# Kernel tuning notes

Hardware: AMD Instinct MI355X
Metric: run time of the kernel (lower is better)

Reference implementation:

```python
import jax, jax.numpy as jnp
import numpy as np


def _gcn(G, A, x, W, b):
    # G: (K,N,N) chebyshev supports, A: (B,N,N) attention, x: (B,N,p)
    s = jnp.einsum('kij,bjp->bkip', G, x)          # graph conv per cheb order
    s = jnp.einsum('bij,bkjp->bikp', A, s)         # attention bmm, -> (B,N,K,p)
    B, N, K, p = s.shape
    s = s.reshape(B, N, K * p)                     # concat over k (k-major blocks)
    return s @ W + b


def setup_inputs() -> dict:
    key = jax.random.key(0)
    ks = jax.random.split(key, 8)
    B, T, N, C = 16, 12, 1024, 1
    K, H = 3, 64
    din = C + H  # 65
    x = jax.random.normal(ks[0], (B, T, N, C), dtype=jnp.float32)
    G = jax.random.normal(ks[1], (K, N, N), dtype=jnp.float32) / np.sqrt(N)
    A = jax.random.uniform(ks[2], (B, N, N), dtype=jnp.float32) / N
    W_gate = jax.random.normal(ks[3], (K * din, 2 * H), dtype=jnp.float32) * 0.02
    b_gate = jnp.zeros((2 * H,), dtype=jnp.float32)
    W_update = jax.random.normal(ks[4], (K * din, H), dtype=jnp.float32) * 0.02
    b_update = jnp.zeros((H,), dtype=jnp.float32)
    W_dec = jax.random.normal(ks[5], (H, 12 * 1), dtype=jnp.float32) * 0.02
    b_dec = jnp.zeros((12,), dtype=jnp.float32)
    return {"x": x, "G": G, "A": A, "W_gate": W_gate, "b_gate": b_gate,
            "W_update": W_update, "b_update": b_update, "W_dec": W_dec, "b_dec": b_dec}


def reference(x, G, A, W_gate, b_gate, W_update, b_update, W_dec, b_dec):
    B, T, N, _ = x.shape
    H = W_update.shape[1]
    out_steps, output_dim = 12, 1

    def step(h, xt):
        combined = jnp.concatenate([xt, h], axis=-1)              # (B,N,din)
        zr = jax.nn.sigmoid(_gcn(G, A, combined, W_gate, b_gate))  # (B,N,2H)
        z, r = zr[..., :H], zr[..., H:]
        cand = jnp.concatenate([xt, r * h], axis=-1)
        hc = jnp.tanh(_gcn(G, A, cand, W_update, b_update))
        h_new = z * hc + (1.0 - z) * h
        return h_new, None

    h0 = jnp.zeros((B, N, H), dtype=x.dtype)
    h_last, _ = jax.lax.scan(step, h0, jnp.swapaxes(x, 0, 1))      # scan over T
    out = h_last @ W_dec + b_dec                                   # (B,N,out_steps*output_dim)
    out = out.reshape(B, N, out_steps, output_dim)
    return jnp.transpose(out, (0, 2, 1, 3))                        # (B,out_steps,N,output_dim)
```

## Files before the change

kernel.cpp:

```cpp
#include <hip/hip_runtime.h>

#define B_  16
#define T_  12
#define N_  1024
#define K_  3
#define H_  64
#define DIN 65
#define KH  192
#define OG  128

typedef _Float16 f16x4 __attribute__((ext_vector_type(4)));
typedef _Float16 f16x8 __attribute__((ext_vector_type(8)));
typedef float    f32x4 __attribute__((ext_vector_type(4)));

static const size_t OFF_H   = 0;
static const size_t OFF_ZB  = 1048576;
static const size_t OFF_S2  = 2097152;
static const size_t OFF_HTA = 2686976;
static const size_t OFF_HTB = 3211264;
static const size_t OFF_S1  = 3735552;
static const size_t OFF_WGT = 4030464;
static const size_t OFF_WUT = 4042752;
static const size_t OFF_WX  = 4048896;
static const size_t OFF_GT  = 4049472;
static const size_t OFF_AG  = 5622336;
static const size_t OFF_AF  = 30788160;

__global__ __launch_bounds__(256) void k_repack(const float* __restrict__ Wg,
                                                const float* __restrict__ Wu,
                                                _Float16* __restrict__ wghT,
                                                _Float16* __restrict__ wuhT,
                                                float* __restrict__ wx) {
    const float inv = 1.0f / 1024.0f;
    int idx = blockIdx.x * 256 + threadIdx.x;
    if (idx < 128 * 192) {
        int o = idx / 192, d = idx % 192;
        int k = d / 64, c = d % 64;
        wghT[idx] = (_Float16)(Wg[(size_t)(k * DIN + 1 + c) * OG + o] * inv);
    } else if (idx < 128 * 192 + 64 * 192) {
        int j = idx - 128 * 192;
        int o = j / 192, d = j % 192;
        int k = d / 64, c = d % 64;
        wuhT[j] = (_Float16)(Wu[(size_t)(k * DIN + 1 + c) * H_ + o] * inv);
    } else if (idx < 128 * 192 + 64 * 192 + 576) {
        int j = idx - 128 * 192 - 64 * 192;
        if (j < 384) { int k = j >> 7, o = j & 127; wx[j] = Wg[(size_t)(k * DIN) * OG + o] * inv; }
        else { int j2 = j - 384; int k = j2 >> 6, o = j2 & 63; wx[j] = Wu[(size_t)(k * DIN) * H_ + o] * inv; }
    }
}

__global__ __launch_bounds__(256) void k_acvt(const float* __restrict__ A,
                                              _Float16* __restrict__ Af) {
    size_t idx = ((size_t)blockIdx.x * 256 + threadIdx.x) * 8;
    float4 a = *(const float4*)&A[idx];
    float4 c = *(const float4*)&A[idx + 4];
    f16x8 v = {(_Float16)(a.x*1024.f), (_Float16)(a.y*1024.f), (_Float16)(a.z*1024.f), (_Float16)(a.w*1024.f),
               (_Float16)(c.x*1024.f), (_Float16)(c.y*1024.f), (_Float16)(c.z*1024.f), (_Float16)(c.w*1024.f)};
    *(f16x8*)&Af[idx] = v;
}

__global__ __launch_bounds__(256) void k_gtr(const float* __restrict__ G,
                                             _Float16* __restrict__ GfT) {
    int bx = blockIdx.x;
    int kk = bx >> 8, rem = bx & 255, ti = rem >> 4, tj = rem & 15;
    int i0 = ti * 64, j0 = tj * 64;
    __shared__ _Float16 s[64][72];
    int tid = threadIdx.x;
    int r = tid >> 2, cb = (tid & 3) * 16;
    const float* Gp = G + ((size_t)kk << 20) + ((size_t)(i0 + r) << 10) + j0 + cb;
    #pragma unroll
    for (int q = 0; q < 4; ++q) {
        float4 v = *(const float4*)&Gp[q * 4];
        f16x4 hv = {(_Float16)v.x, (_Float16)v.y, (_Float16)v.z, (_Float16)v.w};
        *(f16x4*)&s[r][cb + q * 4] = hv;
    }
    __syncthreads();
    alignas(16) _Float16 tmp[16];
    #pragma unroll
    for (int q = 0; q < 16; ++q) tmp[q] = s[cb + q][r];
    _Float16* outp = GfT + ((size_t)kk << 20) + ((size_t)(j0 + r) << 10) + i0 + cb;
    *(f16x8*)&outp[0] = *(f16x8*)&tmp[0];
    *(f16x8*)&outp[8] = *(f16x8*)&tmp[8];
}

__global__ __launch_bounds__(256) void k_ag(const _Float16* __restrict__ Af,
                                            const _Float16* __restrict__ GfT,
                                            _Float16* __restrict__ AG) {
    int bxr = blockIdx.x;
    int bx = (bxr & 7) * 384 + (bxr >> 3);
    int inst = bx >> 6, tile = bx & 63;
    int b = inst / 3, kk = inst % 3;
    int i0 = (tile >> 3) * 128, j0 = (tile & 7) * 128;
    __shared__ _Float16 sA[2][128][72], sB[2][128][72];
    int tid = threadIdx.x;
    int w = tid >> 6, lane = tid & 63, ln = lane & 15, kg = lane >> 4;
    int mq = (w & 1) * 64, nq = (w >> 1) * 64;
    int srow = tid >> 1, cb = (tid & 1) * 32;
    const _Float16* qa = Af  + ((size_t)b << 20)  + ((size_t)(i0 + srow) << 10) + cb;
    const _Float16* qb = GfT + ((size_t)kk << 20) + ((size_t)(j0 + srow) << 10) + cb;

    f32x4 acc[4][4];
    #pragma unroll
    for (int mt = 0; mt < 4; ++mt)
        #pragma unroll
        for (int nt = 0; nt < 4; ++nt) acc[mt][nt] = (f32x4){0.f, 0.f, 0.f, 0.f};

    f16x8 ra[4], rb[4];
    #pragma unroll
    for (int q = 0; q < 4; ++q) { ra[q] = *(const f16x8*)&qa[q * 8]; rb[q] = *(const f16x8*)&qb[q * 8]; }
    #pragma unroll
    for (int q = 0; q < 4; ++q) {
        *(f16x8*)&sA[0][srow][cb + q * 8] = ra[q];
        *(f16x8*)&sB[0][srow][cb + q * 8] = rb[q];
    }
    __syncthreads();

    for (int tt = 0; tt < 16; ++tt) {
        int cur = tt & 1;
        if (tt < 15) {
            int kn = (tt + 1) * 64;
            #pragma unroll
            for (int q = 0; q < 4; ++q) { ra[q] = *(const f16x8*)&qa[kn + q * 8]; rb[q] = *(const f16x8*)&qb[kn + q * 8]; }
        }
        #pragma unroll
        for (int ks = 0; ks < 2; ++ks) {
            int ko = ks * 32 + kg * 8;
            f16x8 a[4], bfr[4];
            #pragma unroll
            for (int mt = 0; mt < 4; ++mt) a[mt] = *(const f16x8*)&sA[cur][mq + mt * 16 + ln][ko];
            #pragma unroll
            for (int nt = 0; nt < 4; ++nt) bfr[nt] = *(const f16x8*)&sB[cur][nq + nt * 16 + ln][ko];
            #pragma unroll
            for (int mt = 0; mt < 4; ++mt)
                #pragma unroll
                for (int nt = 0; nt < 4; ++nt)
                    acc[mt][nt] = __builtin_amdgcn_mfma_f32_16x16x32_f16(a[mt], bfr[nt], acc[mt][nt], 0, 0, 0);
        }
        if (tt < 15) {
            int nb = cur ^ 1;
            #pragma unroll
            for (int q = 0; q < 4; ++q) {
                *(f16x8*)&sA[nb][srow][cb + q * 8] = ra[q];
                *(f16x8*)&sB[nb][srow][cb + q * 8] = rb[q];
            }
            __syncthreads();
        }
    }

    _Float16* outp = AG + ((size_t)(b * 3 + kk) << 20);
    #pragma unroll
    for (int mt = 0; mt < 4; ++mt)
        #pragma unroll
        for (int r = 0; r < 4; ++r) {
            int i = i0 + mq + mt * 16 + kg * 4 + r;
            #pragma unroll
            for (int nt = 0; nt < 4; ++nt) {
                int j = j0 + nq + nt * 16 + ln;
                outp[((size_t)i << 10) + j] = (_Float16)acc[mt][nt][r];
            }
        }
}

__global__ __launch_bounds__(256) void k_s1b(const float* __restrict__ G,
                                             const float* __restrict__ x,
                                             _Float16* __restrict__ S1) {
    int bx = blockIdx.x;
    int nh = bx & 1, it = (bx >> 1) & 15, kk = bx >> 5;
    int i0 = it * 64, m0 = nh * 96;
    __shared__ _Float16 sA[64][72], sB[96][72];
    int tid = threadIdx.x, wid = tid >> 6, ln = tid & 15, kl = (tid & 63) >> 4;
    const float* Gk = G + (size_t)kk * N_ * N_;
    f32x4 acc[6];
    #pragma unroll
    for (int n = 0; n < 6; ++n) acc[n] = (f32x4){0.f, 0.f, 0.f, 0.f};
    for (int kc = 0; kc < N_; kc += 64) {
        #pragma unroll
        for (int it2 = 0; it2 < 4; ++it2) {
            int idx = it2 * 256 + tid; int row = idx >> 4, c4 = (idx & 15) * 4;
            float4 g = *(const float4*)&Gk[(size_t)(i0 + row) * N_ + kc + c4];
            f16x4 hv = {(_Float16)g.x, (_Float16)g.y, (_Float16)g.z, (_Float16)g.w};
            *(f16x4*)&sA[row][c4] = hv;
        }
        #pragma unroll
        for (int it2 = 0; it2 < 6; ++it2) {
            int idx = it2 * 256 + tid; int row = idx >> 4, c4 = (idx & 15) * 4;
            float4 g = *(const float4*)&x[(size_t)(m0 + row) * N_ + kc + c4];
            f16x4 hv = {(_Float16)g.x, (_Float16)g.y, (_Float16)g.z, (_Float16)g.w};
            *(f16x4*)&sB[row][c4] = hv;
        }
        __syncthreads();
        #pragma unroll
        for (int ks = 0; ks < 4; ++ks) {
            int ko = ks * 16 + kl * 4;
            f16x4 a = *(const f16x4*)&sA[wid * 16 + ln][ko];
            #pragma unroll
            for (int n = 0; n < 6; ++n) {
                f16x4 b = *(const f16x4*)&sB[n * 16 + ln][ko];
                acc[n] = __builtin_amdgcn_mfma_f32_16x16x16f16(a, b, acc[n], 0, 0, 0);
            }
        }
        __syncthreads();
    }
    #pragma unroll
    for (int n = 0; n < 6; ++n) {
        int m = m0 + n * 16 + ln;
        #pragma unroll
        for (int r = 0; r < 4; ++r) {
            int i = i0 + wid * 16 + kl * 4 + r;
            S1[(((size_t)kk * 192 + m) << 10) + i] = (_Float16)acc[n][r];
        }
    }
}

__global__ __launch_bounds__(256) void k_s2b(const _Float16* __restrict__ Af,
                                             const _Float16* __restrict__ S1,
                                             float* __restrict__ S2) {
    int bx = blockIdx.x; int it = bx & 15, b = bx >> 4; int i0 = it * 64;
    __shared__ _Float16 sA[64][72], sB[48][72];
    int tid = threadIdx.x, wid = tid >> 6, ln = tid & 15, kl = (tid & 63) >> 4;
    f32x4 acc[3];
    #pragma unroll
    for (int n = 0; n < 3; ++n) acc[n] = (f32x4){0.f, 0.f, 0.f, 0.f};
    for (int kc = 0; kc < N_; kc += 64) {
        #pragma unroll
        for (int it2 = 0; it2 < 2; ++it2) {
            int idx = it2 * 256 + tid; int row = idx >> 3, c8 = (idx & 7) * 8;
            *(uint4*)&sA[row][c8] = *(const uint4*)&Af[((size_t)b << 20) + ((size_t)(i0 + row) << 10) + kc + c8];
        }
        for (int idx = tid; idx < 288; idx += 256) {
            int row = idx >> 3, c8 = (idx & 7) * 8;
            int kq = row / 12, tq = row - kq * 12;
            *(uint4*)&sB[row][c8] = *(const uint4*)&S1[(((size_t)kq * 192 + b * T_ + tq) << 10) + kc + c8];
        }
        __syncthreads();
        #pragma unroll
        for (int ks = 0; ks < 4; ++ks) {
            int ko = ks * 16 + kl * 4;
            f16x4 a = *(const f16x4*)&sA[wid * 16 + ln][ko];
            #pragma unroll
            for (int n = 0; n < 3; ++n) {
                f16x4 b = *(const f16x4*)&sB[n * 16 + ln][ko];
                acc[n] = __builtin_amdgcn_mfma_f32_16x16x16f16(a, b, acc[n], 0, 0, 0);
            }
        }
        __syncthreads();
    }
    #pragma unroll
    for (int n = 0; n < 3; ++n) {
        int col = n * 16 + ln;
        if (col < 36) {
            int kq = col / 12, tq = col - kq * 12;
            #pragma unroll
            for (int r = 0; r < 4; ++r) {
                int i = i0 + wid * 16 + kl * 4 + r;
                S2[(((size_t)(b * 3 + kq) * T_ + tq) << 10) + i] = acc[n][r];
            }
        }
    }
}

__global__ __launch_bounds__(256) void k_fzr(const _Float16* __restrict__ AG,
                                             const _Float16* __restrict__ HtIn,
                                             const _Float16* __restrict__ wghT,
                                             const float* __restrict__ wx,
                                             const float* __restrict__ bg,
                                             const float* __restrict__ S2,
                                             const float* __restrict__ h,
                                             float* __restrict__ zb,
                                             _Float16* __restrict__ HtOut, int t) {
    int bx = blockIdx.x; int it = bx & 63, b = bx >> 6; int i0 = it * 16;
    __shared__ __align__(16) char smem[32256];
    _Float16 (*sA)[48][72] = reinterpret_cast<_Float16(*)[48][72]>(smem);
    _Float16 (*sB)[64][72] = reinterpret_cast<_Float16(*)[64][72]>(smem + 13824);
    _Float16 (*sZ)[200]    = reinterpret_cast<_Float16(*)[200]>(smem);
    _Float16 (*sW)[72]     = reinterpret_cast<_Float16(*)[72]>(smem + 6400);
    __shared__ float sS2[3][16];
    __shared__ float sWX[384];
    __shared__ float sBias[128];
    int tid = threadIdx.x;
    int w = tid >> 6, lane = tid & 63, ln = lane & 15, kg = lane >> 4;
    if (tid < 48) { int k = tid >> 4, il = tid & 15; sS2[k][il] = S2[(((size_t)(b * 3 + k) * T_ + t) << 10) + i0 + il]; }
    for (int q = tid; q < 384; q += 256) sWX[q] = wx[q];
    if (tid < 128) sBias[tid] = bg[tid];

    const _Float16* pA[3]; int c4A[3], rowA[3];
    #pragma unroll
    for (int q = 0; q < 3; ++q) {
        int idx = q * 256 + tid; rowA[q] = idx >> 4; c4A[q] = (idx & 15) * 4;
        int kb = rowA[q] >> 4, rloc = rowA[q] & 15;
        pA[q] = AG + ((size_t)(b * 3 + kb) << 20) + ((size_t)(i0 + rloc) << 10) + c4A[q];
    }
    const _Float16* pB[2]; int c8B[2], rowB[2];
    #pragma unroll
    for (int q = 0; q < 2; ++q) {
        int idx = q * 256 + tid; rowB[q] = idx >> 3; c8B[q] = (idx & 7) * 8;
        pB[q] = HtIn + ((size_t)b << 16) + ((size_t)rowB[q] << 10) + c8B[q];
    }

    f32x4 acc[3];
    #pragma unroll
    for (int n = 0; n < 3; ++n) acc[n] = (f32x4){0.f, 0.f, 0.f, 0.f};

    f16x4 ra[3]; f16x8 rb[2];
    #pragma unroll
    for (int q = 0; q < 3; ++q) ra[q] = *(const f16x4*)pA[q];
    #pragma unroll
    for (int q = 0; q < 2; ++q) rb[q] = *(const f16x8*)pB[q];
    #pragma unroll
    for (int q = 0; q < 3; ++q) *(f16x4*)&sA[0][rowA[q]][c4A[q]] = ra[q];
    #pragma unroll
    for (int q = 0; q < 2; ++q) *(f16x8*)&sB[0][rowB[q]][c8B[q]] = rb[q];
    __syncthreads();

    int kbF = (w * 3) >> 2, kbL = (w * 3 + 2) >> 2;
    for (int tt = 0; tt < 16; ++tt) {
        int cur = tt & 1;
        if (tt < 15) {
            int kn = (tt + 1) * 64;
            #pragma unroll
            for (int q = 0; q < 3; ++q) ra[q] = *(const f16x4*)&pA[q][kn];
            #pragma unroll
            for (int q = 0; q < 2; ++q) rb[q] = *(const f16x8*)&pB[q][kn];
        }
        #pragma unroll
        for (int ks = 0; ks < 2; ++ks) {
            int ko = ks * 32 + kg * 8;
            f16x8 aF = *(const f16x8*)&sA[cur][kbF * 16 + ln][ko];
            f16x8 aL = *(const f16x8*)&sA[cur][kbL * 16 + ln][ko];
            #pragma unroll
            for (int ni = 0; ni < 3; ++ni) {
                int ct = w * 3 + ni;
                f16x8 bb = *(const f16x8*)&sB[cur][(ct & 3) * 16 + ln][ko];
                f16x8 a = ((ct >> 2) != kbF) ? aL : aF;
                acc[ni] = __builtin_amdgcn_mfma_f32_16x16x32_f16(a, bb, acc[ni], 0, 0, 0);
            }
        }
        if (tt < 15) {
            int nb = cur ^ 1;
            #pragma unroll
            for (int q = 0; q < 3; ++q) *(f16x4*)&sA[nb][rowA[q]][c4A[q]] = ra[q];
            #pragma unroll
            for (int q = 0; q < 2; ++q) *(f16x8*)&sB[nb][rowB[q]][c8B[q]] = rb[q];
            __syncthreads();
        }
    }
    __syncthreads();

    #pragma unroll
    for (int ni = 0; ni < 3; ++ni)
        #pragma unroll
        for (int r = 0; r < 4; ++r)
            sZ[kg * 4 + r][(w * 3 + ni) * 16 + ln] = (_Float16)acc[ni][r];

    f32x4 e[2];
    e[0] = (f32x4){0.f, 0.f, 0.f, 0.f};
    e[1] = (f32x4){0.f, 0.f, 0.f, 0.f};
    for (int kc = 0; kc < 192; kc += 64) {
        #pragma unroll
        for (int it2 = 0; it2 < 4; ++it2) {
            int idx = it2 * 256 + tid; int row = idx >> 3, c8 = (idx & 7) * 8;
            *(f16x8*)&sW[row][c8] = *(const f16x8*)&wghT[(size_t)row * 192 + kc + c8];
        }
        __syncthreads();
        #pragma unroll
        for (int ks = 0; ks < 4; ++ks) {
            int ko = ks * 16 + kg * 4;
            f16x4 az  = *(const f16x4*)&sZ[ln][kc + ko];
            f16x4 bw0 = *(const f16x4*)&sW[w * 32 + ln][ko];
            f16x4 bw1 = *(const f16x4*)&sW[w * 32 + 16 + ln][ko];
            e[0] = __builtin_amdgcn_mfma_f32_16x16x16f16(az, bw0, e[0], 0, 0, 0);
            e[1] = __builtin_amdgcn_mfma_f32_16x16x16f16(az, bw1, e[1], 0, 0, 0);
        }
        __syncthreads();
    }

    #pragma unroll
    for (int n = 0; n < 2; ++n) {
        int o = w * 32 + n * 16 + ln;
        float w0 = sWX[o], w1 = sWX[128 + o], w2 = sWX[256 + o], bi = sBias[o];
        if (o < H_) {
            #pragma unroll
            for (int r = 0; r < 4; ++r) {
                int il = kg * 4 + r;
                float pre = e[n][r] + w0 * sS2[0][il] + w1 * sS2[1][il] + w2 * sS2[2][il] + bi;
                float v = 1.0f / (1.0f + expf(-pre));
                zb[((size_t)((b << 10) + i0 + il)) * H_ + o] = v;
            }
        } else {
            int c = o - H_;
            alignas(8) _Float16 hb[4];
            #pragma unroll
            for (int r = 0; r < 4; ++r) {
                int il = kg * 4 + r;
                float pre = e[n][r] + w0 * sS2[0][il] + w1 * sS2[1][il] + w2 * sS2[2][il] + bi;
                float v = 1.0f / (1.0f + expf(-pre));
                hb[r] = (_Float16)(v * h[((size_t)((b << 10) + i0 + il)) * H_ + c]);
            }
            *(f16x4*)&HtOut[((size_t)(b * 64 + c) << 10) + i0 + kg * 4] = *(f16x4*)&hb[0];
        }
    }
}

__global__ __launch_bounds__(256) void k_fup(const _Float16* __restrict__ AG,
                                             const _Float16* __restrict__ HtIn,
                                             const _Float16* __restrict__ wuhT,
                                             const float* __restrict__ wx,
                                             const float* __restrict__ bu,
                                             const float* __restrict__ S2,
                                             const float* __restrict__ zb,
                                             float* __restrict__ h,
                                             _Float16* __restrict__ HtOut, int t) {
    int bx = blockIdx.x; int it = bx & 63, b = bx >> 6; int i0 = it * 16;
    __shared__ __align__(16) char smem[32256];
    _Float16 (*sA)[48][72] = reinterpret_cast<_Float16(*)[48][72]>(smem);
    _Float16 (*sB)[64][72] = reinterpret_cast<_Float16(*)[64][72]>(smem + 13824);
    _Float16 (*sZ)[200]    = reinterpret_cast<_Float16(*)[200]>(smem);
    _Float16 (*sW)[72]     = reinterpret_cast<_Float16(*)[72]>(smem + 6400);
    __shared__ float sS2[3][16];
    __shared__ float sWX[192];
    __shared__ float sBias[64];
    int tid = threadIdx.x;
    int w = tid >> 6, lane = tid & 63, ln = lane & 15, kg = lane >> 4;
    if (tid < 48) { int k = tid >> 4, il = tid & 15; sS2[k][il] = S2[(((size_t)(b * 3 + k) * T_ + t) << 10) + i0 + il]; }
    if (tid < 192) sWX[tid] = wx[384 + tid];
    if (tid < 64) sBias[tid] = bu[tid];

    const _Float16* pA[3]; int c4A[3], rowA[3];
    #pragma unroll
    for (int q = 0; q < 3; ++q) {
        int idx = q * 256 + tid; rowA[q] = idx >> 4; c4A[q] = (idx & 15) * 4;
        int kb = rowA[q] >> 4, rloc = rowA[q] & 15;
        pA[q] = AG + ((size_t)(b * 3 + kb) << 20) + ((size_t)(i0 + rloc) << 10) + c4A[q];
    }
    const _Float16* pB[2]; int c8B[2], rowB[2];
    #pragma unroll
    for (int q = 0; q < 2; ++q) {
        int idx = q * 256 + tid; rowB[q] = idx >> 3; c8B[q] = (idx & 7) * 8;
        pB[q] = HtIn + ((size_t)b << 16) + ((size_t)rowB[q] << 10) + c8B[q];
    }

    f32x4 acc[3];
    #pragma unroll
    for (int n = 0; n < 3; ++n) acc[n] = (f32x4){0.f, 0.f, 0.f, 0.f};

    f16x4 ra[3]; f16x8 rb[2];
    #pragma unroll
    for (int q = 0; q < 3; ++q) ra[q] = *(const f16x4*)pA[q];
    #pragma unroll
    for (int q = 0; q < 2; ++q) rb[q] = *(const f16x8*)pB[q];
    #pragma unroll
    for (int q = 0; q < 3; ++q) *(f16x4*)&sA[0][rowA[q]][c4A[q]] = ra[q];
    #pragma unroll
    for (int q = 0; q < 2; ++q) *(f16x8*)&sB[0][rowB[q]][c8B[q]] = rb[q];
    __syncthreads();

    int kbF = (w * 3) >> 2, kbL = (w * 3 + 2) >> 2;
    for (int tt = 0; tt < 16; ++tt) {
        int cur = tt & 1;
        if (tt < 15) {
            int kn = (tt + 1) * 64;
            #pragma unroll
            for (int q = 0; q < 3; ++q) ra[q] = *(const f16x4*)&pA[q][kn];
            #pragma unroll
            for (int q = 0; q < 2; ++q) rb[q] = *(const f16x8*)&pB[q][kn];
        }
        #pragma unroll
        for (int ks = 0; ks < 2; ++ks) {
            int ko = ks * 32 + kg * 8;
            f16x8 aF = *(const f16x8*)&sA[cur][kbF * 16 + ln][ko];
            f16x8 aL = *(const f16x8*)&sA[cur][kbL * 16 + ln][ko];
            #pragma unroll
            for (int ni = 0; ni < 3; ++ni) {
                int ct = w * 3 + ni;
                f16x8 bb = *(const f16x8*)&sB[cur][(ct & 3) * 16 + ln][ko];
                f16x8 a = ((ct >> 2) != kbF) ? aL : aF;
                acc[ni] = __builtin_amdgcn_mfma_f32_16x16x32_f16(a, bb, acc[ni], 0, 0, 0);
            }
        }
        if (tt < 15) {
            int nb = cur ^ 1;
            #pragma unroll
            for (int q = 0; q < 3; ++q) *(f16x4*)&sA[nb][rowA[q]][c4A[q]] = ra[q];
            #pragma unroll
            for (int q = 0; q < 2; ++q) *(f16x8*)&sB[nb][rowB[q]][c8B[q]] = rb[q];
            __syncthreads();
        }
    }
    __syncthreads();

    #pragma unroll
    for (int ni = 0; ni < 3; ++ni)
        #pragma unroll
        for (int r = 0; r < 4; ++r)
            sZ[kg * 4 + r][(w * 3 + ni) * 16 + ln] = (_Float16)acc[ni][r];

    f32x4 e = (f32x4){0.f, 0.f, 0.f, 0.f};
    for (int kc = 0; kc < 192; kc += 64) {
        #pragma unroll
        for (int it2 = 0; it2 < 2; ++it2) {
            int idx = it2 * 256 + tid; int row = idx >> 3, c8 = (idx & 7) * 8;
            *(f16x8*)&sW[row][c8] = *(const f16x8*)&wuhT[(size_t)row * 192 + kc + c8];
        }
        __syncthreads();
        #pragma unroll
        for (int ks = 0; ks < 4; ++ks) {
            int ko = ks * 16 + kg * 4;
            f16x4 az = *(const f16x4*)&sZ[ln][kc + ko];
            f16x4 bw = *(const f16x4*)&sW[w * 16 + ln][ko];
            e = __builtin_amdgcn_mfma_f32_16x16x16f16(az, bw, e, 0, 0, 0);
        }
        __syncthreads();
    }

    int o = w * 16 + ln;
    float w0 = sWX[o], w1 = sWX[64 + o], w2 = sWX[128 + o], bi = sBias[o];
    alignas(8) _Float16 hb[4];
    #pragma unroll
    for (int r = 0; r < 4; ++r) {
        int il = kg * 4 + r;
        float pre = e[r] + w0 * sS2[0][il] + w1 * sS2[1][il] + w2 * sS2[2][il] + bi;
        float hc = tanhf(pre);
        size_t gi = ((size_t)((b << 10) + i0 + il)) * H_ + o;
        float z = zb[gi], hold = h[gi];
        float hn = z * hc + (1.0f - z) * hold;
        h[gi] = hn;
        hb[r] = (_Float16)hn;
    }
    *(f16x4*)&HtOut[((size_t)(b * 64 + o) << 10) + i0 + kg * 4] = *(f16x4*)&hb[0];
}

__global__ __launch_bounds__(256) void k_dec(const float* __restrict__ h,
                                             const float* __restrict__ Wd,
                                             const float* __restrict__ bd,
                                             float* __restrict__ out) {
    int bx = blockIdx.x;
    int b = bx >> 4, it = bx & 15; int i0 = it * 64;
    __shared__ float hs[64][65];
    __shared__ float Wds[64][12];
    __shared__ float bds[12];
    int tid = threadIdx.x;
    for (int idx = tid; idx < 4096; idx += 256) {
        int r = idx >> 6, c = idx & 63;
        hs[r][c] = h[(size_t)(b * N_ + i0 + r) * H_ + c];
    }
    for (int idx = tid; idx < 768; idx += 256)
        Wds[idx / 12][idx % 12] = Wd[idx];
    if (tid < 12) bds[tid] = bd[tid];
    __syncthreads();
    for (int oidx = tid; oidx < 768; oidx += 256) {
        int i = oidx & 63, tt = oidx >> 6;
        float acc = bds[tt];
        #pragma unroll
        for (int c = 0; c < 64; ++c) acc += hs[i][c] * Wds[c][tt];
        out[(size_t)(b * T_ + tt) * N_ + i0 + i] = acc;
    }
}

extern "C" void kernel_launch(void* const* d_in, const int* in_sizes, int n_in,
                              void* d_out, int out_size, void* d_ws, size_t ws_size,
                              hipStream_t stream) {
    const float* x  = (const float*)d_in[0];
    const float* G  = (const float*)d_in[1];
    const float* A  = (const float*)d_in[2];
    const float* Wg = (const float*)d_in[3];
    const float* bg = (const float*)d_in[4];
    const float* Wu = (const float*)d_in[5];
    const float* bu = (const float*)d_in[6];
    const float* Wd = (const float*)d_in[7];
    const float* bd = (const float*)d_in[8];
    float* out = (float*)d_out;
    float* ws  = (float*)d_ws;

    float* h   = ws + OFF_H;
    float* zb  = ws + OFF_ZB;
    float* S2  = ws + OFF_S2;
    float* wxb = ws + OFF_WX;
    _Float16* HtA  = (_Float16*)(ws + OFF_HTA);
    _Float16* HtB  = (_Float16*)(ws + OFF_HTB);
    _Float16* S1   = (_Float16*)(ws + OFF_S1);
    _Float16* wghT = (_Float16*)(ws + OFF_WGT);
    _Float16* wuhT = (_Float16*)(ws + OFF_WUT);
    _Float16* GfT  = (_Float16*)(ws + OFF_GT);
    _Float16* AG   = (_Float16*)(ws + OFF_AG);
    _Float16* Af   = (_Float16*)(ws + OFF_AF);

    hipMemsetAsync(h, 0, (size_t)B_ * N_ * H_ * sizeof(float), stream);
    hipMemsetAsync((void*)HtA, 0, (size_t)B_ * N_ * H_ * sizeof(_Float16), stream);
    k_repack<<<147, 256, 0, stream>>>(Wg, Wu, wghT, wuhT, wxb);
    k_gtr<<<768, 256, 0, stream>>>(G, GfT);
    k_acvt<<<8192, 256, 0, stream>>>(A, Af);
    k_ag<<<3072, 256, 0, stream>>>(Af, GfT, AG);
    k_s1b<<<96, 256, 0, stream>>>(G, x, S1);
    k_s2b<<<256, 256, 0, stream>>>(Af, S1, S2);

    for (int t = 0; t < T_; ++t) {
        k_fzr<<<1024, 256, 0, stream>>>(AG, HtA, wghT, wxb, bg, S2, h, zb, HtB, t);
        k_fup<<<1024, 256, 0, stream>>>(AG, HtB, wuhT, wxb, bu, S2, zb, h, HtA, t);
    }
    k_dec<<<256, 256, 0, stream>>>(h, Wd, bd, out);
}
```

Before: 823.3 us.

## Fuse recurrent timesteps into a persistent cooperative kernel with grid sync

Merges the preprocessing kernels (A/G conversion, G transpose, weight repack, S1) into one launch and the AG and S2 GEMMs into a second. The 24 per-timestep launches become a single cooperative persistent kernel of 512 blocks that synchronises the grid between phases, with the decoder folded into the final step. Gate z is stored as fp16 in a transposed layout instead of fp32, and a launch-per-step fallback is kept for when occupancy is too low. This removes launch overhead and inter-kernel gaps, but grid-wide barriers add cost and only 512 blocks may underuse the device.

```diff
diff --git a/kernel.cpp b/kernel.cpp
--- a/kernel.cpp
+++ b/kernel.cpp
@@ -1,4 +1,7 @@
 #include <hip/hip_runtime.h>
+#include <hip/hip_cooperative_groups.h>
+
+namespace cg = cooperative_groups;
 
 #define B_  16
 #define T_  12
@@ -14,7 +17,7 @@
 typedef float    f32x4 __attribute__((ext_vector_type(4)));
 
 static const size_t OFF_H   = 0;
-static const size_t OFF_ZB  = 1048576;
+static const size_t OFF_ZF  = 1048576;
 static const size_t OFF_S2  = 2097152;
 static const size_t OFF_HTA = 2686976;
 static const size_t OFF_HTB = 3211264;
@@ -26,248 +29,483 @@
 static const size_t OFF_AG  = 5622336;
 static const size_t OFF_AF  = 30788160;
 
-__global__ __launch_bounds__(256) void k_repack(const float* __restrict__ Wg,
-                                                const float* __restrict__ Wu,
-                                                _Float16* __restrict__ wghT,
-                                                _Float16* __restrict__ wuhT,
-                                                float* __restrict__ wx) {
-    const float inv = 1.0f / 1024.0f;
-    int idx = blockIdx.x * 256 + threadIdx.x;
-    if (idx < 128 * 192) {
-        int o = idx / 192, d = idx % 192;
-        int k = d / 64, c = d % 64;
-        wghT[idx] = (_Float16)(Wg[(size_t)(k * DIN + 1 + c) * OG + o] * inv);
-    } else if (idx < 128 * 192 + 64 * 192) {
-        int j = idx - 128 * 192;
-        int o = j / 192, d = j % 192;
-        int k = d / 64, c = d % 64;
-        wuhT[j] = (_Float16)(Wu[(size_t)(k * DIN + 1 + c) * H_ + o] * inv);
-    } else if (idx < 128 * 192 + 64 * 192 + 576) {
-        int j = idx - 128 * 192 - 64 * 192;
-        if (j < 384) { int k = j >> 7, o = j & 127; wx[j] = Wg[(size_t)(k * DIN) * OG + o] * inv; }
-        else { int j2 = j - 384; int k = j2 >> 6, o = j2 & 63; wx[j] = Wu[(size_t)(k * DIN) * H_ + o] * inv; }
+__global__ __launch_bounds__(256) void k_pre(const float* __restrict__ A,
+                                             const float* __restrict__ G,
+                                             const float* __restrict__ x,
+                                             const float* __restrict__ Wg,
+                                             const float* __restrict__ Wu,
+                                             _Float16* __restrict__ Af,
+                                             _Float16* __restrict__ GfT,
+                                             _Float16* __restrict__ S1,
+                                             _Float16* __restrict__ wghT,
+                                             _Float16* __restrict__ wuhT,
+                                             float* __restrict__ wx) {
+    __shared__ __align__(16) char smem[23040];
+    int bx0 = blockIdx.x, tid = threadIdx.x;
+    if (bx0 < 96) {
+        int bx = bx0;
+        int nh = bx & 1, it = (bx >> 1) & 15, kk = bx >> 5;
+        int i0 = it * 64, m0 = nh * 96;
+        _Float16 (*sA)[72] = reinterpret_cast<_Float16(*)[72]>(smem);
+        _Float16 (*sB)[72] = reinterpret_cast<_Float16(*)[72]>(smem + 9216);
+        int wid = tid >> 6, ln = tid & 15, kl = (tid & 63) >> 4;
+        const float* Gk = G + (size_t)kk * N_ * N_;
+        f32x4 acc[6];
+        #pragma unroll
+        for (int n = 0; n < 6; ++n) acc[n] = (f32x4){0.f, 0.f, 0.f, 0.f};
+        for (int kc = 0; kc < N_; kc += 64) {
+            #pragma unroll
+            for (int it2 = 0; it2 < 4; ++it2) {
+                int idx = it2 * 256 + tid; int row = idx >> 4, c4 = (idx & 15) * 4;
+                float4 g = *(const float4*)&Gk[(size_t)(i0 + row) * N_ + kc + c4];
+                f16x4 hv = {(_Float16)g.x, (_Float16)g.y, (_Float16)g.z, (_Float16)g.w};
+                *(f16x4*)&sA[row][c4] = hv;
+            }
+            #pragma unroll
+            for (int it2 = 0; it2 < 6; ++it2) {
+                int idx = it2 * 256 + tid; int row = idx >> 4, c4 = (idx & 15) * 4;
+                float4 g = *(const float4*)&x[(size_t)(m0 + row) * N_ + kc + c4];
+                f16x4 hv = {(_Float16)g.x, (_Float16)g.y, (_Float16)g.z, (_Float16)g.w};
+                *(f16x4*)&sB[row][c4] = hv;
+            }
+            __syncthreads();
+            #pragma unroll
+            for (int ks = 0; ks < 4; ++ks) {
+                int ko = ks * 16 + kl * 4;
+                f16x4 a = *(const f16x4*)&sA[wid * 16 + ln][ko];
+                #pragma unroll
+                for (int n = 0; n < 6; ++n) {
+                    f16x4 b = *(const f16x4*)&sB[n * 16 + ln][ko];
+                    acc[n] = __builtin_amdgcn_mfma_f32_16x16x16f16(a, b, acc[n], 0, 0, 0);
+                }
+            }
+            __syncthreads();
+        }
+        #pragma unroll
+        for (int n = 0; n < 6; ++n) {
+            int m = m0 + n * 16 + ln;
+            #pragma unroll
+            for (int r = 0; r < 4; ++r) {
+                int i = i0 + wid * 16 + kl * 4 + r;
+                S1[(((size_t)kk * 192 + m) << 10) + i] = (_Float16)acc[n][r];
+            }
+        }
+    } else if (bx0 < 864) {
+        int bx = bx0 - 96;
+        int kk = bx >> 8, rem = bx & 255, ti = rem >> 4, tj = rem & 15;
+        int i0 = ti * 64, j0 = tj * 64;
+        _Float16 (*s)[72] = reinterpret_cast<_Float16(*)[72]>(smem);
+        int r = tid >> 2, cb = (tid & 3) * 16;
+        const float* Gp = G + ((size_t)kk << 20) + ((size_t)(i0 + r) << 10) + j0 + cb;
+        #pragma unroll
+        for (int q = 0; q < 4; ++q) {
+            float4 v = *(const float4*)&Gp[q * 4];
+            f16x4 hv = {(_Float16)v.x, (_Float16)v.y, (_Float16)v.z, (_Float16)v.w};
+            *(f16x4*)&s[r][cb + q * 4] = hv;
+        }
+        __syncthreads();
+        alignas(16) _Float16 tmp[16];
+        #pragma unroll
+        for (int q = 0; q < 16; ++q) tmp[q] = s[cb + q][r];
+        _Float16* outp = GfT + ((size_t)kk << 20) + ((size_t)(j0 + r) << 10) + i0 + cb;
+        *(f16x8*)&outp[0] = *(f16x8*)&tmp[0];
+        *(f16x8*)&outp[8] = *(f16x8*)&tmp[8];
+    } else if (bx0 < 1011) {
+        const float inv = 1.0f / 1024.0f;
+        int idx = (bx0 - 864) * 256 + tid;
+        if (idx < 128 * 192) {
+            int o = idx / 192, d = idx % 192;
+            int k = d / 64, c = d % 64;
+            wghT[idx] = (_Float16)(Wg[(size_t)(k * DIN + 1 + c) * OG + o] * inv);
+        } else if (idx < 128 * 192 + 64 * 192) {
+            int j = idx - 128 * 192;
+            int o = j / 192, d = j % 192;
+            int k = d / 64, c = d % 64;
+            wuhT[j] = (_Float16)(Wu[(size_t)(k * DIN + 1 + c) * H_ + o] * inv);
+        } else if (idx < 128 * 192 + 64 * 192 + 576) {
+            int j = idx - 128 * 192 - 64 * 192;
+            if (j < 384) { int k = j >> 7, o = j & 127; wx[j] = Wg[(size_t)(k * DIN) * OG + o] * inv; }
+            else { int j2 = j - 384; int k = j2 >> 6, o = j2 & 63; wx[j] = Wu[(size_t)(k * DIN) * H_ + o] * inv; }
+        }
+    } else {
+        size_t idx = ((size_t)(bx0 - 1011) * 256 + tid) * 8;
+        float4 a = *(const float4*)&A[idx];
+        float4 c = *(const float4*)&A[idx + 4];
+        f16x8 v = {(_Float16)(a.x*1024.f), (_Float16)(a.y*1024.f), (_Float16)(a.z*1024.f), (_Float16)(a.w*1024.f),
+                   (_Float16)(c.x*1024.f), (_Float16)(c.y*1024.f), (_Float16)(c.z*1024.f), (_Float16)(c.w*1024.f)};
+        *(f16x8*)&Af[idx] = v;
     }
 }
 
-__global__ __launch_bounds__(256) void k_acvt(const float* __restrict__ A,
-                                              _Float16* __restrict__ Af) {
-    size_t idx = ((size_t)blockIdx.x * 256 + threadIdx.x) * 8;
-    float4 a = *(const float4*)&A[idx];
-    float4 c = *(const float4*)&A[idx + 4];
-    f16x8 v = {(_Float16)(a.x*1024.f), (_Float16)(a.y*1024.f), (_Float16)(a.z*1024.f), (_Float16)(a.w*1024.f),
-               (_Float16)(c.x*1024.f), (_Float16)(c.y*1024.f), (_Float16)(c.z*1024.f), (_Float16)(c.w*1024.f)};
-    *(f16x8*)&Af[idx] = v;
+__global__ __launch_bounds__(256) void k_main(const _Float16* __restrict__ Af,
+                                              const _Float16* __restrict__ GfT,
+                                              _Float16* __restrict__ AG,
+                                              const _Float16* __restrict__ S1,
+                                              float* __restrict__ S2) {
+    __shared__ __align__(16) char smem[73728];
+    int bx0 = blockIdx.x, tid = threadIdx.x;
+    if (bx0 < 256) {
+        int bx = bx0; int it = bx & 15, b = bx >> 4; int i0 = it * 64;
+        _Float16 (*sA)[72] = reinterpret_cast<_Float16(*)[72]>(smem);
+        _Float16 (*sB)[72] = reinterpret_cast<_Float16(*)[72]>(smem + 9216);
+        int wid = tid >> 6, ln = tid & 15, kl = (tid & 63) >> 4;
+        f32x4 acc[3];
+        #pragma unroll
+        for (int n = 0; n < 3; ++n) acc[n] = (f32x4){0.f, 0.f, 0.f, 0.f};
+        for (int kc = 0; kc < N_; kc += 64) {
+            #pragma unroll
+            for (int it2 = 0; it2 < 2; ++it2) {
+                int idx = it2 * 256 + tid; int row = idx >> 3, c8 = (idx & 7) * 8;
+                *(uint4*)&sA[row][c8] = *(const uint4*)&Af[((size_t)b << 20) + ((size_t)(i0 + row) << 10) + kc + c8];
+            }
+            for (int idx = tid; idx < 288; idx += 256) {
+                int row = idx >> 3, c8 = (idx & 7) * 8;
+                int kq = row / 12, tq = row - kq * 12;
+                *(uint4*)&sB[row][c8] = *(const uint4*)&S1[(((size_t)kq * 192 + b * T_ + tq) << 10) + kc + c8];
+            }
+            __syncthreads();
+            #pragma unroll
+            for (int ks = 0; ks < 4; ++ks) {
+                int ko = ks * 16 + kl * 4;
+                f16x4 a = *(const f16x4*)&sA[wid * 16 + ln][ko];
+                #pragma unroll
+                for (int n = 0; n < 3; ++n) {
+                    f16x4 b = *(const f16x4*)&sB[n * 16 + ln][ko];
+                    acc[n] = __builtin_amdgcn_mfma_f32_16x16x16f16(a, b, acc[n], 0, 0, 0);
+                }
+            }
+            __syncthreads();
+        }
+        #pragma unroll
+        for (int n = 0; n < 3; ++n) {
+            int col = n * 16 + ln;
+            if (col < 36) {
+                int kq = col / 12, tq = col - kq * 12;
+                #pragma unroll
+                for (int r = 0; r < 4; ++r) {
+                    int i = i0 + wid * 16 + kl * 4 + r;
+                    S2[(((size_t)(b * 3 + kq) * T_ + tq) << 10) + i] = acc[n][r];
+                }
+            }
+        }
+    } else {
+        int bxr = bx0 - 256;
+        int bx = (bxr & 7) * 384 + (bxr >> 3);
+        int inst = bx >> 6, tile = bx & 63;
+        int b = inst / 3, kk = inst % 3;
+        int i0 = (tile >> 3) * 128, j0 = (tile & 7) * 128;
+        _Float16 (*sA)[128][72] = reinterpret_cast<_Float16(*)[128][72]>(smem);
+        _Float16 (*sB)[128][72] = reinterpret_cast<_Float16(*)[128][72]>(smem + 36864);
+        int w = tid >> 6, lane = tid & 63, ln = lane & 15, kg = lane >> 4;
+        int mq = (w & 1) * 64, nq = (w >> 1) * 64;
+        int srow = tid >> 1, cb = (tid & 1) * 32;
+        const _Float16* qa = Af  + ((size_t)b << 20)  + ((size_t)(i0 + srow) << 10) + cb;
+        const _Float16* qb = GfT + ((size_t)kk << 20) + ((size_t)(j0 + srow) << 10) + cb;
+
+        f32x4 acc[4][4];
+        #pragma unroll
+        for (int mt = 0; mt < 4; ++mt)
+            #pragma unroll
+            for (int nt = 0; nt < 4; ++nt) acc[mt][nt] = (f32x4){0.f, 0.f, 0.f, 0.f};
+
+        f16x8 ra[4], rb[4];
+        #pragma unroll
+        for (int q = 0; q < 4; ++q) { ra[q] = *(const f16x8*)&qa[q * 8]; rb[q] = *(const f16x8*)&qb[q * 8]; }
+        #pragma unroll
+        for (int q = 0; q < 4; ++q) {
+            *(f16x8*)&sA[0][srow][cb + q * 8] = ra[q];
+            *(f16x8*)&sB[0][srow][cb + q * 8] = rb[q];
+        }
+        __syncthreads();
+
+        for (int tt = 0; tt < 16; ++tt) {
+            int cur = tt & 1;
+            if (tt < 15) {
+                int kn = (tt + 1) * 64;
+                #pragma unroll
+                for (int q = 0; q < 4; ++q) { ra[q] = *(const f16x8*)&qa[kn + q * 8]; rb[q] = *(const f16x8*)&qb[kn + q * 8]; }
+            }
+            #pragma unroll
+            for (int ks = 0; ks < 2; ++ks) {
+                int ko = ks * 32 + kg * 8;
+                f16x8 a[4], bfr[4];
+                #pragma unroll
+                for (int mt = 0; mt < 4; ++mt) a[mt] = *(const f16x8*)&sA[cur][mq + mt * 16 + ln][ko];
+                #pragma unroll
+                for (int nt = 0; nt < 4; ++nt) bfr[nt] = *(const f16x8*)&sB[cur][nq + nt * 16 + ln][ko];
+                #pragma unroll
+                for (int mt = 0; mt < 4; ++mt)
+                    #pragma unroll
+                    for (int nt = 0; nt < 4; ++nt)
+                        acc[mt][nt] = __builtin_amdgcn_mfma_f32_16x16x32_f16(a[mt], bfr[nt], acc[mt][nt], 0, 0, 0);
+            }
+            if (tt < 15) {
+                int nb = cur ^ 1;
+                #pragma unroll
+                for (int q = 0; q < 4; ++q) {
+                    *(f16x8*)&sA[nb][srow][cb + q * 8] = ra[q];
+                    *(f16x8*)&sB[nb][srow][cb + q * 8] = rb[q];
+                }
+                __syncthreads();
+            }
+        }
+
+        _Float16* outp = AG + ((size_t)(b * 3 + kk) << 20);
+        #pragma unroll
+        for (int mt = 0; mt < 4; ++mt)
+            #pragma unroll
+            for (int r = 0; r < 4; ++r) {
+                int i = i0 + mq + mt * 16 + kg * 4 + r;
+                #pragma unroll
+                for (int nt = 0; nt < 4; ++nt) {
+                    int j = j0 + nq + nt * 16 + ln;
+                    outp[((size_t)i << 10) + j] = (_Float16)acc[mt][nt][r];
+                }
+            }
+    }
 }
 
-__global__ __launch_bounds__(256) void k_gtr(const float* __restrict__ G,
-                                             _Float16* __restrict__ GfT) {
-    int bx = blockIdx.x;
-    int kk = bx >> 8, rem = bx & 255, ti = rem >> 4, tj = rem & 15;
-    int i0 = ti * 64, j0 = tj * 64;
-    __shared__ _Float16 s[64][72];
-    int tid = threadIdx.x;
-    int r = tid >> 2, cb = (tid & 3) * 16;
-    const float* Gp = G + ((size_t)kk << 20) + ((size_t)(i0 + r) << 10) + j0 + cb;
-    #pragma unroll
-    for (int q = 0; q < 4; ++q) {
-        float4 v = *(const float4*)&Gp[q * 4];
-        f16x4 hv = {(_Float16)v.x, (_Float16)v.y, (_Float16)v.z, (_Float16)v.w};
-        *(f16x4*)&s[r][cb + q * 4] = hv;
-    }
-    __syncthreads();
-    alignas(16) _Float16 tmp[16];
-    #pragma unroll
-    for (int q = 0; q < 16; ++q) tmp[q] = s[cb + q][r];
-    _Float16* outp = GfT + ((size_t)kk << 20) + ((size_t)(j0 + r) << 10) + i0 + cb;
-    *(f16x8*)&outp[0] = *(f16x8*)&tmp[0];
-    *(f16x8*)&outp[8] = *(f16x8*)&tmp[8];
-}
-
-__global__ __launch_bounds__(256) void k_ag(const _Float16* __restrict__ Af,
-                                            const _Float16* __restrict__ GfT,
-                                            _Float16* __restrict__ AG) {
-    int bxr = blockIdx.x;
-    int bx = (bxr & 7) * 384 + (bxr >> 3);
-    int inst = bx >> 6, tile = bx & 63;
-    int b = inst / 3, kk = inst % 3;
-    int i0 = (tile >> 3) * 128, j0 = (tile & 7) * 128;
-    __shared__ _Float16 sA[2][128][72], sB[2][128][72];
+__global__ __launch_bounds__(256, 2) void k_loop(const _Float16* __restrict__ AG,
+                                                 _Float16* __restrict__ HtA,
+                                                 _Float16* __restrict__ HtB,
+                                                 const _Float16* __restrict__ wghT,
+                                                 const _Float16* __restrict__ wuhT,
+                                                 const float* __restrict__ wx,
+                                                 const float* __restrict__ bg,
+                                                 const float* __restrict__ bu,
+                                                 const float* __restrict__ S2,
+                                                 const float* __restrict__ Wd,
+                                                 const float* __restrict__ bd,
+                                                 float* __restrict__ out) {
+    cg::grid_group grid = cg::this_grid();
+    int bx = blockIdx.x; int it = bx & 31, b = bx >> 5; int i0 = it * 32;
+    __shared__ __align__(16) char smem[46080];
+    _Float16 (*sAm)[96][72] = reinterpret_cast<_Float16(*)[96][72]>(smem);
+    _Float16 (*sBm)[64][72] = reinterpret_cast<_Float16(*)[64][72]>(smem + 27648);
+    _Float16 (*sZ)[200]     = reinterpret_cast<_Float16(*)[200]>(smem);
+    _Float16 (*sW)[72]      = reinterpret_cast<_Float16(*)[72]>(smem + 12800);
+    __shared__ _Float16 zS[32][64];
+    __shared__ float sS2[3][32];
     int tid = threadIdx.x;
     int w = tid >> 6, lane = tid & 63, ln = lane & 15, kg = lane >> 4;
-    int mq = (w & 1) * 64, nq = (w >> 1) * 64;
-    int srow = tid >> 1, cb = (tid & 1) * 32;
-    const _Float16* qa = Af  + ((size_t)b << 20)  + ((size_t)(i0 + srow) << 10) + cb;
-    const _Float16* qb = GfT + ((size_t)kk << 20) + ((size_t)(j0 + srow) << 10) + cb;
-
-    f32x4 acc[4][4];
-    #pragma unroll
-    for (int mt = 0; mt < 4; ++mt)
-        #pragma unroll
-        for (int nt = 0; nt < 4; ++nt) acc[mt][nt] = (f32x4){0.f, 0.f, 0.f, 0.f};
-
-    f16x8 ra[4], rb[4];
-    #pragma unroll
-    for (int q = 0; q < 4; ++q) { ra[q] = *(const f16x8*)&qa[q * 8]; rb[q] = *(const f16x8*)&qb[q * 8]; }
-    #pragma unroll
-    for (int q = 0; q < 4; ++q) {
-        *(f16x8*)&sA[0][srow][cb + q * 8] = ra[q];
-        *(f16x8*)&sB[0][srow][cb + q * 8] = rb[q];
-    }
+
+    float h_reg[2][4] = {{0.f, 0.f, 0.f, 0.f}, {0.f, 0.f, 0.f, 0.f}};
+    float wxg0[2], wxg1[2], wxg2[2], bgr[2];
+    #pragma unroll
+    for (int n = 0; n < 2; ++n) {
+        int o = w * 32 + n * 16 + ln;
+        wxg0[n] = wx[o]; wxg1[n] = wx[128 + o]; wxg2[n] = wx[256 + o]; bgr[n] = bg[o];
+    }
+    int ou = w * 16 + ln;
+    float wxu0 = wx[384 + ou], wxu1 = wx[448 + ou], wxu2 = wx[512 + ou], bur = bu[ou];
+
+    int srow = tid >> 3, sc8 = (tid & 7) * 8;
+    const _Float16* pa0 = AG + ((size_t)(b * 3 + 0) << 20) + ((size_t)(i0 + srow) << 10) + sc8;
+    const _Float16* pa1 = AG + ((size_t)(b * 3 + 1) << 20) + ((size_t)(i0 + srow) << 10) + sc8;
+    const _Float16* pa2 = AG + ((size_t)(b * 3 + 2) << 20) + ((size_t)(i0 + srow) << 10) + sc8;
+    size_t hoff0 = ((size_t)b << 16) + ((size_t)srow << 10) + sc8;
+    size_t hoff1 = ((size_t)b << 16) + ((size_t)(srow + 32) << 10) + sc8;
+    int kbF = (w * 3) >> 2, kbL = (w * 3 + 2) >> 2;
+
+    for (int t = 0; t < T_; ++t) {
+        #pragma unroll
+        for (int phase = 0; phase < 2; ++phase) {
+            const _Float16* HtIn = phase ? HtB : HtA;
+            if (tid < 96) { int k = tid >> 5, il = tid & 31; sS2[k][il] = S2[(((size_t)(b * 3 + k) * T_ + t) << 10) + i0 + il]; }
+            const _Float16* pb0 = HtIn + hoff0;
+            const _Float16* pb1 = HtIn + hoff1;
+
+            f32x4 acc[2][3];
+            #pragma unroll
+            for (int m = 0; m < 2; ++m)
+                #pragma unroll
+                for (int n = 0; n < 3; ++n) acc[m][n] = (f32x4){0.f, 0.f, 0.f, 0.f};
+
+            f16x8 rA0 = *(const f16x8*)pa0, rA1 = *(const f16x8*)pa1, rA2 = *(const f16x8*)pa2;
+            f16x8 rB0 = *(const f16x8*)pb0, rB1 = *(const f16x8*)pb1;
+            *(f16x8*)&sAm[0][srow][sc8] = rA0;
+            *(f16x8*)&sAm[0][32 + srow][sc8] = rA1;
+            *(f16x8*)&sAm[0][64 + srow][sc8] = rA2;
+            *(f16x8*)&sBm[0][srow][sc8] = rB0;
+            *(f16x8*)&sBm[0][srow + 32][sc8] = rB1;
+            __syncthreads();
+
+            for (int tt = 0; tt < 16; ++tt) {
+                int cur = tt & 1;
+                if (tt < 15) {
+                    int kn = (tt + 1) * 64;
+                    rA0 = *(const f16x8*)&pa0[kn]; rA1 = *(const f16x8*)&pa1[kn]; rA2 = *(const f16x8*)&pa2[kn];
+                    rB0 = *(const f16x8*)&pb0[kn]; rB1 = *(const f16x8*)&pb1[kn];
+                }
+                #pragma unroll
+                for (int ks = 0; ks < 2; ++ks) {
+                    int ko = ks * 32 + kg * 8;
+                    f16x8 aF0 = *(const f16x8*)&sAm[cur][kbF * 32 + ln][ko];
+                    f16x8 aF1 = *(const f16x8*)&sAm[cur][kbF * 32 + 16 + ln][ko];
+                    f16x8 aL0 = *(const f16x8*)&sAm[cur][kbL * 32 + ln][ko];
+                    f16x8 aL1 = *(const f16x8*)&sAm[cur][kbL * 32 + 16 + ln][ko];
+                    #pragma unroll
+                    for (int ni = 0; ni < 3; ++ni) {
+                        int ct = w * 3 + ni;
+                        f16x8 bb = *(const f16x8*)&sBm[cur][(ct & 3) * 16 + ln][ko];
+                        bool late = (ct >> 2) != kbF;
+                        f16x8 a0 = late ? aL0 : aF0;
+                        f16x8 a1 = late ? aL1 : aF1;
+                        acc[0][ni] = __builtin_amdgcn_mfma_f32_16x16x32_f16(a0, bb, acc[0][ni], 0, 0, 0);
+                        acc[1][ni] = __builtin_amdgcn_mfma_f32_16x16x32_f16(a1, bb, acc[1][ni], 0, 0, 0);
+                    }
+                }
+                if (tt < 15) {
+                    int nb = cur ^ 1;
+                    *(f16x8*)&sAm[nb][srow][sc8] = rA0;
+                    *(f16x8*)&sAm[nb][32 + srow][sc8] = rA1;
+                    *(f16x8*)&sAm[nb][64 + srow][sc8] = rA2;
+                    *(f16x8*)&sBm[nb][srow][sc8] = rB0;
+                    *(f16x8*)&sBm[nb][srow + 32][sc8] = rB1;
+                    __syncthreads();
+                }
+            }
+            __syncthreads();
+
+            #pragma unroll
+            for (int m = 0; m < 2; ++m)
+                #pragma unroll
+                for (int ni = 0; ni < 3; ++ni)
+                    #pragma unroll
+                    for (int r = 0; r < 4; ++r)
+                        sZ[m * 16 + kg * 4 + r][(w * 3 + ni) * 16 + ln] = (_Float16)acc[m][ni][r];
+
+            if (phase == 0) {
+                f32x4 e[2][2];
+                #pragma unroll
+                for (int m = 0; m < 2; ++m)
+                    #pragma unroll
+                    for (int n = 0; n < 2; ++n) e[m][n] = (f32x4){0.f, 0.f, 0.f, 0.f};
+                for (int kc = 0; kc < 192; kc += 64) {
+                    #pragma unroll
+                    for (int it2 = 0; it2 < 4; ++it2) {
+                        int idx = it2 * 256 + tid; int row = idx >> 3, c8 = (idx & 7) * 8;
+                        *(f16x8*)&sW[row][c8] = *(const f16x8*)&wghT[(size_t)row * 192 + kc + c8];
+                    }
+                    __syncthreads();
+                    #pragma unroll
+                    for (int ks = 0; ks < 4; ++ks) {
+                        int ko = ks * 16 + kg * 4;
+                        f16x4 az0 = *(const f16x4*)&sZ[ln][kc + ko];
+                        f16x4 az1 = *(const f16x4*)&sZ[16 + ln][kc + ko];
+                        f16x4 bw0 = *(const f16x4*)&sW[w * 32 + ln][ko];
+                        f16x4 bw1 = *(const f16x4*)&sW[w * 32 + 16 + ln][ko];
+                        e[0][0] = __builtin_amdgcn_mfma_f32_16x16x16f16(az0, bw0, e[0][0], 0, 0, 0);
+                        e[0][1] = __builtin_amdgcn_mfma_f32_16x16x16f16(az0, bw1, e[0][1], 0, 0, 0);
+                        e[1][0] = __builtin_amdgcn_mfma_f32_16x16x16f16(az1, bw0, e[1][0], 0, 0, 0);
+                        e[1][1] = __builtin_amdgcn_mfma_f32_16x16x16f16(az1, bw1, e[1][1], 0, 0, 0);
+                    }
+                    __syncthreads();
+                }
+                #pragma unroll
+                for (int n = 0; n < 2; ++n) {
+                    int o = w * 32 + n * 16 + ln;
+                    if (o < H_) {
+                        #pragma unroll
+                        for (int m = 0; m < 2; ++m)
+                            #pragma unroll
+                            for (int r = 0; r < 4; ++r) {
+                                int il = m * 16 + kg * 4 + r;
+                                float pre = e[m][n][r] + wxg0[n] * sS2[0][il] + wxg1[n] * sS2[1][il] + wxg2[n] * sS2[2][il] + bgr[n];
+                                zS[il][o] = (_Float16)(1.0f / (1.0f + expf(-pre)));
+                            }
+                    } else {
+                        int c = o - H_;
+                        #pragma unroll
+                        for (int m = 0; m < 2; ++m) {
+                            f16x4 hold4 = *(const f16x4*)&HtA[((size_t)(b * 64 + c) << 10) + i0 + m * 16 + kg * 4];
+                            alignas(8) _Float16 hb[4];
+                            #pragma unroll
+                            for (int r = 0; r < 4; ++r) {
+                                int il = m * 16 + kg * 4 + r;
+                                float pre = e[m][n][r] + wxg0[n] * sS2[0][il] + wxg1[n] * sS2[1][il] + wxg2[n] * sS2[2][il] + bgr[n];
+                                float v = 1.0f / (1.0f + expf(-pre));
+                                hb[r] = (_Float16)(v * (float)hold4[r]);
+                            }
+                            *(f16x4*)&HtB[((size_t)(b * 64 + c) << 10) + i0 + m * 16 + kg * 4] = *(f16x4*)&hb[0];
+                        }
+                    }
+                }
+            } else {
+                f32x4 e[2];
+                e[0] = (f32x4){0.f, 0.f, 0.f, 0.f};
+                e[1] = (f32x4){0.f, 0.f, 0.f, 0.f};
+                for (int kc = 0; kc < 192; kc += 64) {
+                    #pragma unroll
+                    for (int it2 = 0; it2 < 2; ++it2) {
+                        int idx = it2 * 256 + tid; int row = idx >> 3, c8 = (idx & 7) * 8;
+                        *(f16x8*)&sW[row][c8] = *(const f16x8*)&wuhT[(size_t)row * 192 + kc + c8];
+                    }
+                    __syncthreads();
+                    #pragma unroll
+                    for (int ks = 0; ks < 4; ++ks) {
+                        int ko = ks * 16 + kg * 4;
+                        f16x4 az0 = *(const f16x4*)&sZ[ln][kc + ko];
+                        f16x4 az1 = *(const f16x4*)&sZ[16 + ln][kc + ko];
+                        f16x4 bw  = *(const f16x4*)&sW[w * 16 + ln][ko];
+                        e[0] = __builtin_amdgcn_mfma_f32_16x16x16f16(az0, bw, e[0], 0, 0, 0);
+                        e[1] = __builtin_amdgcn_mfma_f32_16x16x16f16(az1, bw, e[1], 0, 0, 0);
+                    }
+                    __syncthreads();
+                }
+                #pragma unroll
+                for (int m = 0; m < 2; ++m) {
+                    alignas(8) _Float16 hb[4];
+                    #pragma unroll
+                    for (int r = 0; r < 4; ++r) {
+                        int il = m * 16 + kg * 4 + r;
+                        float pre = e[m][r] + wxu0 * sS2[0][il] + wxu1 * sS2[1][il] + wxu2 * sS2[2][il] + bur;
+                        float hc = tanhf(pre);
+                        float z = (float)zS[il][ou];
+                        float hn = z * hc + (1.0f - z) * h_reg[m][r];
+                        h_reg[m][r] = hn;
+                        hb[r] = (_Float16)hn;
+                    }
+                    *(f16x4*)&HtA[((size_t)(b * 64 + ou) << 10) + i0 + m * 16 + kg * 4] = *(f16x4*)&hb[0];
+                }
+            }
+            if (t < T_ - 1 || phase == 0) {
+                __threadfence();
+                grid.sync();
+            }
+        }
+    }
+
     __syncthreads();
-
-    for (int tt = 0; tt < 16; ++tt) {
-        int cur = tt & 1;
-        if (tt < 15) {
-            int kn = (tt + 1) * 64;
-            #pragma unroll
-            for (int q = 0; q < 4; ++q) { ra[q] = *(const f16x8*)&qa[kn + q * 8]; rb[q] = *(const f16x8*)&qb[kn + q * 8]; }
-        }
-        #pragma unroll
-        for (int ks = 0; ks < 2; ++ks) {
-            int ko = ks * 32 + kg * 8;
-            f16x8 a[4], bfr[4];
-            #pragma unroll
-            for (int mt = 0; mt < 4; ++mt) a[mt] = *(const f16x8*)&sA[cur][mq + mt * 16 + ln][ko];
-            #pragma unroll
-            for (int nt = 0; nt < 4; ++nt) bfr[nt] = *(const f16x8*)&sB[cur][nq + nt * 16 + ln][ko];
-            #pragma unroll
-            for (int mt = 0; mt < 4; ++mt)
-                #pragma unroll
-                for (int nt = 0; nt < 4; ++nt)
-                    acc[mt][nt] = __builtin_amdgcn_mfma_f32_16x16x32_f16(a[mt], bfr[nt], acc[mt][nt], 0, 0, 0);
-        }
-        if (tt < 15) {
-            int nb = cur ^ 1;
-            #pragma unroll
-            for (int q = 0; q < 4; ++q) {
-                *(f16x8*)&sA[nb][srow][cb + q * 8] = ra[q];
-                *(f16x8*)&sB[nb][srow][cb + q * 8] = rb[q];
-            }
-            __syncthreads();
-        }
-    }
-
-    _Float16* outp = AG + ((size_t)(b * 3 + kk) << 20);
-    #pragma unroll
-    for (int mt = 0; mt < 4; ++mt)
-        #pragma unroll
-        for (int r = 0; r < 4; ++r) {
-            int i = i0 + mq + mt * 16 + kg * 4 + r;
-            #pragma unroll
-            for (int nt = 0; nt < 4; ++nt) {
-                int j = j0 + nq + nt * 16 + ln;
-                outp[((size_t)i << 10) + j] = (_Float16)acc[mt][nt][r];
-            }
-        }
+    float* hF  = (float*)smem;
+    float* wds = (float*)(smem + 8192);
+    float* bds = (float*)(smem + 11264);
+    #pragma unroll
+    for (int m = 0; m < 2; ++m)
+        #pragma unroll
+        for (int r = 0; r < 4; ++r)
+            hF[(m * 16 + kg * 4 + r) * 64 + ou] = h_reg[m][r];
+    for (int idx = tid; idx < 768; idx += 256) wds[idx] = Wd[idx];
+    if (tid < 12) bds[tid] = bd[tid];
+    __syncthreads();
+    for (int oidx = tid; oidx < 384; oidx += 256) {
+        int il = oidx & 31, tt = oidx >> 5;
+        float acc = bds[tt];
+        #pragma unroll
+        for (int c = 0; c < 64; ++c) acc += hF[il * 64 + c] * wds[c * 12 + tt];
+        out[(((size_t)(b * T_ + tt)) << 10) + i0 + il] = acc;
+    }
 }
 
-__global__ __launch_bounds__(256) void k_s1b(const float* __restrict__ G,
-                                             const float* __restrict__ x,
-                                             _Float16* __restrict__ S1) {
-    int bx = blockIdx.x;
-    int nh = bx & 1, it = (bx >> 1) & 15, kk = bx >> 5;
-    int i0 = it * 64, m0 = nh * 96;
-    __shared__ _Float16 sA[64][72], sB[96][72];
-    int tid = threadIdx.x, wid = tid >> 6, ln = tid & 15, kl = (tid & 63) >> 4;
-    const float* Gk = G + (size_t)kk * N_ * N_;
-    f32x4 acc[6];
-    #pragma unroll
-    for (int n = 0; n < 6; ++n) acc[n] = (f32x4){0.f, 0.f, 0.f, 0.f};
-    for (int kc = 0; kc < N_; kc += 64) {
-        #pragma unroll
-        for (int it2 = 0; it2 < 4; ++it2) {
-            int idx = it2 * 256 + tid; int row = idx >> 4, c4 = (idx & 15) * 4;
-            float4 g = *(const float4*)&Gk[(size_t)(i0 + row) * N_ + kc + c4];
-            f16x4 hv = {(_Float16)g.x, (_Float16)g.y, (_Float16)g.z, (_Float16)g.w};
-            *(f16x4*)&sA[row][c4] = hv;
-        }
-        #pragma unroll
-        for (int it2 = 0; it2 < 6; ++it2) {
-            int idx = it2 * 256 + tid; int row = idx >> 4, c4 = (idx & 15) * 4;
-            float4 g = *(const float4*)&x[(size_t)(m0 + row) * N_ + kc + c4];
-            f16x4 hv = {(_Float16)g.x, (_Float16)g.y, (_Float16)g.z, (_Float16)g.w};
-            *(f16x4*)&sB[row][c4] = hv;
-        }
-        __syncthreads();
-        #pragma unroll
-        for (int ks = 0; ks < 4; ++ks) {
-            int ko = ks * 16 + kl * 4;
-            f16x4 a = *(const f16x4*)&sA[wid * 16 + ln][ko];
-            #pragma unroll
-            for (int n = 0; n < 6; ++n) {
-                f16x4 b = *(const f16x4*)&sB[n * 16 + ln][ko];
-                acc[n] = __builtin_amdgcn_mfma_f32_16x16x16f16(a, b, acc[n], 0, 0, 0);
-            }
-        }
-        __syncthreads();
-    }
-    #pragma unroll
-    for (int n = 0; n < 6; ++n) {
-        int m = m0 + n * 16 + ln;
-        #pragma unroll
-        for (int r = 0; r < 4; ++r) {
-            int i = i0 + wid * 16 + kl * 4 + r;
-            S1[(((size_t)kk * 192 + m) << 10) + i] = (_Float16)acc[n][r];
-        }
-    }
-}
-
-__global__ __launch_bounds__(256) void k_s2b(const _Float16* __restrict__ Af,
-                                             const _Float16* __restrict__ S1,
-                                             float* __restrict__ S2) {
-    int bx = blockIdx.x; int it = bx & 15, b = bx >> 4; int i0 = it * 64;
-    __shared__ _Float16 sA[64][72], sB[48][72];
-    int tid = threadIdx.x, wid = tid >> 6, ln = tid & 15, kl = (tid & 63) >> 4;
-    f32x4 acc[3];
-    #pragma unroll
-    for (int n = 0; n < 3; ++n) acc[n] = (f32x4){0.f, 0.f, 0.f, 0.f};
-    for (int kc = 0; kc < N_; kc += 64) {
-        #pragma unroll
-        for (int it2 = 0; it2 < 2; ++it2) {
-            int idx = it2 * 256 + tid; int row = idx >> 3, c8 = (idx & 7) * 8;
-            *(uint4*)&sA[row][c8] = *(const uint4*)&Af[((size_t)b << 20) + ((size_t)(i0 + row) << 10) + kc + c8];
-        }
-        for (int idx = tid; idx < 288; idx += 256) {
-            int row = idx >> 3, c8 = (idx & 7) * 8;
-            int kq = row / 12, tq = row - kq * 12;
-            *(uint4*)&sB[row][c8] = *(const uint4*)&S1[(((size_t)kq * 192 + b * T_ + tq) << 10) + kc + c8];
-        }
-        __syncthreads();
-        #pragma unroll
-        for (int ks = 0; ks < 4; ++ks) {
-            int ko = ks * 16 + kl * 4;
-            f16x4 a = *(const f16x4*)&sA[wid * 16 + ln][ko];
-            #pragma unroll
-            for (int n = 0; n < 3; ++n) {
-                f16x4 b = *(const f16x4*)&sB[n * 16 + ln][ko];
-                acc[n] = __builtin_amdgcn_mfma_f32_16x16x16f16(a, b, acc[n], 0, 0, 0);
-            }
-        }
-        __syncthreads();
-    }
-    #pragma unroll
-    for (int n = 0; n < 3; ++n) {
-        int col = n * 16 + ln;
-        if (col < 36) {
-            int kq = col / 12, tq = col - kq * 12;
-            #pragma unroll
-            for (int r = 0; r < 4; ++r) {
-                int i = i0 + wid * 16 + kl * 4 + r;
-                S2[(((size_t)(b * 3 + kq) * T_ + tq) << 10) + i] = acc[n][r];
-            }
-        }
-    }
-}
-
-__global__ __launch_bounds__(256) void k_fzr(const _Float16* __restrict__ AG,
-                                             const _Float16* __restrict__ HtIn,
-                                             const _Float16* __restrict__ wghT,
-                                             const float* __restrict__ wx,
-                                             const float* __restrict__ bg,
-                                             const float* __restrict__ S2,
-                                             const float* __restrict__ h,
-                                             float* __restrict__ zb,
-                                             _Float16* __restrict__ HtOut, int t) {
+__global__ __launch_bounds__(256) void k_fzr2(const _Float16* __restrict__ AG,
+                                              const _Float16* __restrict__ HtIn,
+                                              const _Float16* __restrict__ wghT,
+                                              const float* __restrict__ wx,
+                                              const float* __restrict__ bg,
+                                              const float* __restrict__ S2,
+                                              const float* __restrict__ h,
+                                              _Float16* __restrict__ zf,
+                                              _Float16* __restrict__ HtOut, int t) {
     int bx = blockIdx.x; int it = bx & 63, b = bx >> 6; int i0 = it * 16;
     __shared__ __align__(16) char smem[32256];
     _Float16 (*sA)[48][72] = reinterpret_cast<_Float16(*)[48][72]>(smem);
@@ -379,13 +617,14 @@
         int o = w * 32 + n * 16 + ln;
         float w0 = sWX[o], w1 = sWX[128 + o], w2 = sWX[256 + o], bi = sBias[o];
         if (o < H_) {
+            alignas(8) _Float16 zv[4];
             #pragma unroll
             for (int r = 0; r < 4; ++r) {
                 int il = kg * 4 + r;
                 float pre = e[n][r] + w0 * sS2[0][il] + w1 * sS2[1][il] + w2 * sS2[2][il] + bi;
-                float v = 1.0f / (1.0f + expf(-pre));
-                zb[((size_t)((b << 10) + i0 + il)) * H_ + o] = v;
-            }
+                zv[r] = (_Float16)(1.0f / (1.0f + expf(-pre)));
+            }
+            *(f16x4*)&zf[((size_t)(b * 64 + o) << 10) + i0 + kg * 4] = *(f16x4*)&zv[0];
         } else {
             int c = o - H_;
             alignas(8) _Float16 hb[4];
@@ -401,15 +640,18 @@
     }
 }
 
-__global__ __launch_bounds__(256) void k_fup(const _Float16* __restrict__ AG,
-                                             const _Float16* __restrict__ HtIn,
-                                             const _Float16* __restrict__ wuhT,
-                                             const float* __restrict__ wx,
-                                             const float* __restrict__ bu,
-                                             const float* __restrict__ S2,
-                                             const float* __restrict__ zb,
-                                             float* __restrict__ h,
-                                             _Float16* __restrict__ HtOut, int t) {
+__global__ __launch_bounds__(256) void k_fup2(const _Float16* __restrict__ AG,
+                                              const _Float16* __restrict__ HtIn,
+                                              const _Float16* __restrict__ wuhT,
+                                              const float* __restrict__ wx,
+                                              const float* __restrict__ bu,
+                                              const float* __restrict__ S2,
+                                              const _Float16* __restrict__ zf,
+                                              float* __restrict__ h,
+                                              _Float16* __restrict__ HtOut,
+                                              const float* __restrict__ Wd,
+                                              const float* __restrict__ bd,
+                                              float* __restrict__ out, int t) {
     int bx = blockIdx.x; int it = bx & 63, b = bx >> 6; int i0 = it * 16;
     __shared__ __align__(16) char smem[32256];
     _Float16 (*sA)[48][72] = reinterpret_cast<_Float16(*)[48][72]>(smem);
@@ -514,45 +756,40 @@
 
     int o = w * 16 + ln;
     float w0 = sWX[o], w1 = sWX[64 + o], w2 = sWX[128 + o], bi = sBias[o];
+    f16x4 z4 = *(const f16x4*)&zf[((size_t)(b * 64 + o) << 10) + i0 + kg * 4];
     alignas(8) _Float16 hb[4];
+    float hnv[4];
     #pragma unroll
     for (int r = 0; r < 4; ++r) {
         int il = kg * 4 + r;
         float pre = e[r] + w0 * sS2[0][il] + w1 * sS2[1][il] + w2 * sS2[2][il] + bi;
         float hc = tanhf(pre);
         size_t gi = ((size_t)((b << 10) + i0 + il)) * H_ + o;
-        float z = zb[gi], hold = h[gi];
-        float hn = z * hc + (1.0f - z) * hold;
+        float z = (float)z4[r];
+        float hn = z * hc + (1.0f - z) * h[gi];
         h[gi] = hn;
+        hnv[r] = hn;
         hb[r] = (_Float16)hn;
     }
     *(f16x4*)&HtOut[((size_t)(b * 64 + o) << 10) + i0 + kg * 4] = *(f16x4*)&hb[0];
-}
-
-__global__ __launch_bounds__(256) void k_dec(const float* __restrict__ h,
-                                             const float* __restrict__ Wd,
-                                             const float* __restrict__ bd,
-                                             float* __restrict__ out) {
-    int bx = blockIdx.x;
-    int b = bx >> 4, it = bx & 15; int i0 = it * 64;
-    __shared__ float hs[64][65];
-    __shared__ float Wds[64][12];
-    __shared__ float bds[12];
-    int tid = threadIdx.x;
-    for (int idx = tid; idx < 4096; idx += 256) {
-        int r = idx >> 6, c = idx & 63;
-        hs[r][c] = h[(size_t)(b * N_ + i0 + r) * H_ + c];
-    }
-    for (int idx = tid; idx < 768; idx += 256)
-        Wds[idx / 12][idx % 12] = Wd[idx];
-    if (tid < 12) bds[tid] = bd[tid];
-    __syncthreads();
-    for (int oidx = tid; oidx < 768; oidx += 256) {
-        int i = oidx & 63, tt = oidx >> 6;
-        float acc = bds[tt];
-        #pragma unroll
-        for (int c = 0; c < 64; ++c) acc += hs[i][c] * Wds[c][tt];
-        out[(size_t)(b * T_ + tt) * N_ + i0 + i] = acc;
+
+    if (t == T_ - 1) {
+        __syncthreads();
+        float* hF  = (float*)smem;
+        float* wds = (float*)(smem + 4096);
+        float* bds = (float*)(smem + 7168);
+        #pragma unroll
+        for (int r = 0; r < 4; ++r) hF[(kg * 4 + r) * 64 + o] = hnv[r];
+        for (int idx = tid; idx < 768; idx += 256) wds[idx] = Wd[idx];
+        if (tid < 12) bds[tid] = bd[tid];
+        __syncthreads();
+        for (int oidx = tid; oidx < 192; oidx += 256) {
+            int il = oidx & 15, tt2 = oidx >> 4;
+            float acc2 = bds[tt2];
+            #pragma unroll
+            for (int c = 0; c < 64; ++c) acc2 += hF[il * 64 + c] * wds[c * 12 + tt2];
+            out[(((size_t)(b * T_ + tt2)) << 10) + i0 + il] = acc2;
+        }
     }
 }
 
@@ -572,9 +809,9 @@
     float* ws  = (float*)d_ws;
 
     float* h   = ws + OFF_H;
-    float* zb  = ws + OFF_ZB;
     float* S2  = ws + OFF_S2;
     float* wxb = ws + OFF_WX;
+    _Float16* zf   = (_Float16*)(ws + OFF_ZF);
     _Float16* HtA  = (_Float16*)(ws + OFF_HTA);
     _Float16* HtB  = (_Float16*)(ws + OFF_HTB);
     _Float16* S1   = (_Float16*)(ws + OFF_S1);
@@ -586,16 +823,20 @@
 
     hipMemsetAsync(h, 0, (size_t)B_ * N_ * H_ * sizeof(float), stream);
     hipMemsetAsync((void*)HtA, 0, (size_t)B_ * N_ * H_ * sizeof(_Float16), stream);
-    k_repack<<<147, 256, 0, stream>>>(Wg, Wu, wghT, wuhT, wxb);
-    k_gtr<<<768, 256, 0, stream>>>(G, GfT);
-    k_acvt<<<8192, 256, 0, stream>>>(A, Af);
-    k_ag<<<3072, 256, 0, stream>>>(Af, GfT, AG);
-    k_s1b<<<96, 256, 0, stream>>>(G, x, S1);
-    k_s2b<<<256, 256, 0, stream>>>(Af, S1, S2);
-
-    for (int t = 0; t < T_; ++t) {
-        k_fzr<<<1024, 256, 0, stream>>>(AG, HtA, wghT, wxb, bg, S2, h, zb, HtB, t);
-        k_fup<<<1024, 256, 0, stream>>>(AG, HtB, wuhT, wxb, bu, S2, zb, h, HtA, t);
-    }
-    k_dec<<<256, 256, 0, stream>>>(h, Wd, bd, out);
+    k_pre<<<9203, 256, 0, stream>>>(A, G, x, Wg, Wu, Af, GfT, S1, wghT, wuhT, wxb);
+    k_main<<<3328, 256, 0, stream>>>(Af, GfT, AG, S1, S2);
+
+    int nb = 0;
+    hipOccupancyMaxActiveBlocksPerMultiprocessor(&nb, k_loop, 256, 0);
+    if (nb >= 2) {
+        void* args[] = {(void*)&AG, (void*)&HtA, (void*)&HtB, (void*)&wghT, (void*)&wuhT,
+                        (void*)&wxb, (void*)&bg, (void*)&bu, (void*)&S2,
+                        (void*)&Wd, (void*)&bd, (void*)&out};
+        hipLaunchCooperativeKernel((const void*)k_loop, dim3(512), dim3(256), args, 0, stream);
+    } else {
+        for (int t = 0; t < T_; ++t) {
+            k_fzr2<<<1024, 256, 0, stream>>>(AG, HtA, wghT, wxb, bg, S2, h, zf, HtB, t);
+            k_fup2<<<1024, 256, 0, stream>>>(AG, HtB, wuhT, wxb, bu, S2, zf, h, HtA, Wd, bd, out, t);
+        }
+    }
 }
```

After: 799.8 us (median of 3 runs). -2.9%, faster.
